# Kernel optimization log

Measured on AMD Instinct MI355X. Metric: run time of the kernel, lower is better.

## Reference

```python
import jax, jax.numpy as jnp
import numpy as np

B, N, C, H = 8, 1024, 768, 12
D = C // H  # head dim
SCALE = D ** -0.5


def setup_inputs() -> dict:
    key = jax.random.key(0)
    ks = jax.random.split(key, 5)
    return {
        "x": jax.random.normal(ks[0], (B, N, C), dtype=jnp.float32),
        "W_qkv": jax.random.normal(ks[1], (C, 3 * C), dtype=jnp.float32) * (C ** -0.5),
        "b_qkv": jax.random.normal(ks[2], (3 * C,), dtype=jnp.float32) * 0.02,
        "W_proj": jax.random.normal(ks[3], (C, C), dtype=jnp.float32) * (C ** -0.5),
        "b_proj": jax.random.normal(ks[4], (C,), dtype=jnp.float32) * 0.02,
    }


def reference(x, W_qkv, b_qkv, W_proj, b_proj):
    b, n, c = x.shape
    qkv = x @ W_qkv + b_qkv                      # [B,N,3C]
    # rearrange 'b n (k h c) -> k b h n c'
    qkv = qkv.reshape(b, n, 3, H, D).transpose(2, 0, 3, 1, 4)
    q, k, v = qkv[0] * SCALE, qkv[1], qkv[2]     # each [B,H,N,D]
    p = jax.nn.softmax(jnp.einsum('bhnd,bhmd->bhnm', q, k), axis=-1)
    o = jnp.einsum('bhnm,bhmd->bhnd', p, v)      # [B,H,N,D]
    o = o.transpose(0, 2, 1, 3).reshape(b, n, c)  # 'b h n c -> b n (h c)'
    return o @ W_proj + b_proj
```

## Files before the change

### kernel.cpp

```cpp
#include <hip/hip_runtime.h>


typedef short  bf16x8_t __attribute__((ext_vector_type(8)));
typedef float  f32x4_t  __attribute__((ext_vector_type(4)));

static __device__ __forceinline__ unsigned short f2bf(float f) {
    union { float f; unsigned u; } v; v.f = f;
    unsigned r = v.u + 0x7fffu + ((v.u >> 16) & 1u);
    return (unsigned short)(r >> 16);
}

typedef __attribute__((address_space(1))) const unsigned gas_u32;
typedef __attribute__((address_space(3))) unsigned las_u32;
static __device__ __forceinline__ void gload16(const void* g, void* l) {
    __builtin_amdgcn_global_load_lds((gas_u32*)g, (las_u32*)l, 16, 0, 0);
}

#define WAIT0 asm volatile("s_waitcnt vmcnt(0)" ::: "memory")
#define BAR   __builtin_amdgcn_s_barrier()

#define STAGE_TILE(DST, SRC, K0, NP, NT)                                   \
    _Pragma("unroll")                                                      \
    for (int p_ = 0; p_ < NP; ++p_) {                                      \
        const int base_ = p_*NT + wb;                                      \
        const int i_ = base_ + lane;                                       \
        const int row_ = i_ >> 3;                                          \
        const int cb_ = ((i_ & 7) ^ (row_ & 7)) * 8;                       \
        gload16((SRC) + (size_t)row_*768 + (K0) + cb_, &(DST)[base_*8]);   \
    }

#define COMPUTE_P(AS, BS)                                                  \
    {                                                                      \
        bf16x8_t a_[2][2], b_[2][4];                                       \
        _Pragma("unroll")                                                  \
        for (int ks_ = 0; ks_ < 2; ++ks_) {                                \
            _Pragma("unroll")                                              \
            for (int m_ = 0; m_ < 2; ++m_) {                               \
                const int ra_ = wm*32 + m_*16 + l15;                       \
                a_[ks_][m_] = *(const bf16x8_t*)&(AS)[ra_*64 + ((ks_*4 + lhi) ^ (ra_ & 7))*8]; \
            }                                                              \
            _Pragma("unroll")                                              \
            for (int n_ = 0; n_ < 4; ++n_) {                               \
                const int rb_ = wn*64 + n_*16 + l15;                       \
                b_[ks_][n_] = *(const bf16x8_t*)&(BS)[rb_*64 + ((ks_*4 + lhi) ^ (rb_ & 7))*8]; \
            }                                                              \
        }                                                                  \
        _Pragma("unroll")                                                  \
        for (int m_ = 0; m_ < 2; ++m_)                                     \
            _Pragma("unroll")                                              \
            for (int n_ = 0; n_ < 4; ++n_) {                               \
                acc[m_][n_] = __builtin_amdgcn_mfma_f32_16x16x32_bf16(a_[0][m_], b_[0][n_], acc[m_][n_], 0, 0, 0); \
                acc[m_][n_] = __builtin_amdgcn_mfma_f32_16x16x32_bf16(a_[1][m_], b_[1][n_], acc[m_][n_], 0, 0, 0); \
            }                                                              \
    }

#define COMPUTE_Q2(AS, BS)                                                 \
    {                                                                      \
        bf16x8_t a_[2][4], b_[2][2];                                       \
        _Pragma("unroll")                                                  \
        for (int ks_ = 0; ks_ < 2; ++ks_) {                                \
            _Pragma("unroll")                                              \
            for (int m_ = 0; m_ < 4; ++m_) {                               \
                const int ra_ = wm*64 + m_*16 + l15;                       \
                a_[ks_][m_] = *(const bf16x8_t*)&(AS)[ra_*64 + ((ks_*4 + lhi) ^ (ra_ & 7))*8]; \
            }                                                              \
            _Pragma("unroll")                                              \
            for (int n_ = 0; n_ < 2; ++n_) {                               \
                const int rb_ = wn*32 + n_*16 + l15;                       \
                b_[ks_][n_] = *(const bf16x8_t*)&(BS)[rb_*64 + ((ks_*4 + lhi) ^ (rb_ & 7))*8]; \
            }                                                              \
        }                                                                  \
        _Pragma("unroll")                                                  \
        for (int m_ = 0; m_ < 4; ++m_)                                     \
            _Pragma("unroll")                                              \
            for (int n_ = 0; n_ < 2; ++n_) {                               \
                acc[m_][n_] = __builtin_amdgcn_mfma_f32_16x16x32_bf16(a_[0][m_], b_[0][n_], acc[m_][n_], 0, 0, 0); \
                acc[m_][n_] = __builtin_amdgcn_mfma_f32_16x16x32_bf16(a_[1][m_], b_[1][n_], acc[m_][n_], 0, 0, 0); \
            }                                                              \
    }

__global__ __launch_bounds__(256) void convert_x(
    const float* __restrict__ src, unsigned short* __restrict__ dst)
{
    const int i = blockIdx.x * 256 + threadIdx.x;
    const float4 v = ((const float4*)src)[i];
    ushort4 o; o.x = f2bf(v.x); o.y = f2bf(v.y); o.z = f2bf(v.z); o.w = f2bf(v.w);
    ((ushort4*)dst)[i] = o;
}

__global__ __launch_bounds__(256) void transpose_cvt(
    const float* __restrict__ src, unsigned short* __restrict__ dst, int R, int C)
{
    __shared__ unsigned short tile[32][33];
    const int tx = threadIdx.x & 31, ty = threadIdx.x >> 5;
    const int bx = blockIdx.x, by = blockIdx.y;
    #pragma unroll
    for (int j = 0; j < 32; j += 8)
        tile[ty + j][tx] = f2bf(src[(size_t)(by*32 + ty + j) * C + bx*32 + tx]);
    __syncthreads();
    #pragma unroll
    for (int j = 0; j < 32; j += 8)
        dst[(size_t)(bx*32 + ty + j) * R + by*32 + tx] = tile[tx][ty + j];
}

__global__ __launch_bounds__(256, 6) void gemm_qkv_bf16(
    const unsigned short* __restrict__ A, const unsigned short* __restrict__ Bt,
    const float* __restrict__ bias,
    unsigned short* __restrict__ q, unsigned short* __restrict__ kO,
    unsigned short* __restrict__ vT)
{
    __shared__ unsigned short As[128*64];
    __shared__ unsigned short Bs[64*64];
    const int tid = threadIdx.x;
    const int id = blockIdx.x;
    const int xcd = id & 7, r = id >> 3;
    const int nb = r >> 3;
    const int mb = (r & 7) * 8 + xcd;
    const int n0 = nb * 64, m0 = mb * 128;

    const int lane = tid & 63, w = tid >> 6;
    const int l15 = lane & 15, lhi = lane >> 4;
    const int wm = w >> 1, wn = w & 1;
    const int wb = tid & 192;

    const unsigned short* Ab = A  + (size_t)m0 * 768;
    const unsigned short* Bb = Bt + (size_t)n0 * 768;

    f32x4_t acc[4][2] = {};

    #pragma unroll 1
    for (int t = 0; t < 12; ++t) {
        STAGE_TILE(As, Ab, t*64, 4, 256)
        STAGE_TILE(Bs, Bb, t*64, 2, 256)
        WAIT0; BAR;
        COMPUTE_Q2(As, Bs)
        BAR;
    }

    #pragma unroll
    for (int n = 0; n < 2; ++n) {
        const int gcol = n0 + wn*32 + n*16 + l15;
        const int kk = gcol / 768;
        const int rr = gcol - kk*768;
        const int h  = rr >> 6, d = rr & 63;
        const float bv = bias[gcol];
        const float sc = (kk == 0) ? 0.125f : 1.0f;
        #pragma unroll
        for (int m = 0; m < 4; ++m) {
            const int grow_base = m0 + wm*64 + m*16 + lhi*4;
            #pragma unroll
            for (int reg = 0; reg < 4; ++reg) {
                const int grow = grow_base + reg;
                const int bb = grow >> 10, seq = grow & 1023;
                const unsigned short ov = f2bf((acc[m][n][reg] + bv) * sc);
                const size_t bh = (size_t)bb*12 + h;
                if (kk == 0)      q [ (bh*1024 + seq)*64 + d ] = ov;
                else if (kk == 1) kO[ (bh*1024 + seq)*64 + d ] = ov;
                else              vT[ (bh*64 + d)*1024 + seq ] = ov;
            }
        }
    }
}

__global__ __launch_bounds__(512, 6) void attn2(
    const unsigned short* __restrict__ q, const unsigned short* __restrict__ k,
    const unsigned short* __restrict__ vT, unsigned short* __restrict__ obuf)
{
    __shared__ unsigned short Ks[64 * 72];
    __shared__ unsigned short Vs[64 * 72];
    __shared__ unsigned short P[8][16 * 72];
    const int tid = threadIdx.x;
    const int id = blockIdx.x;
    const int swz = (id & 7) * 96 + (id >> 3);
    const int qt = swz & 7, bh = swz >> 3;

    const int lane = tid & 63, w = tid >> 6;
    const int l15 = lane & 15, lhi = lane >> 4;
    const unsigned short* qp = q  + (size_t)bh * 65536;
    const unsigned short* kp = k  + (size_t)bh * 65536;
    const unsigned short* vp = vT + (size_t)bh * 65536;

    bf16x8_t qf[2];
    const int qrow = qt*128 + w*16 + l15;
    #pragma unroll
    for (int ks = 0; ks < 2; ++ks)
        qf[ks] = *(const bf16x8_t*)(qp + (size_t)qrow*64 + ks*32 + lhi*8);

    f32x4_t acco[4] = {};
    float lsum[4] = {0.f, 0.f, 0.f, 0.f};
    unsigned short* Pw = P[w];

    const int r8 = tid >> 3, cb = (tid & 7) * 8;
    bf16x8_t kr, vr;
    kr = *(const bf16x8_t*)(kp + (size_t)r8*64 + cb);
    vr = *(const bf16x8_t*)(vp + (size_t)r8*1024 + cb);
    *(bf16x8_t*)&Ks[r8*72 + cb] = kr;
    *(bf16x8_t*)&Vs[r8*72 + cb] = vr;

    for (int kt = 0; kt < 16; ++kt) {
        __syncthreads();
        if (kt < 15) {
            kr = *(const bf16x8_t*)(kp + (size_t)((kt+1)*64 + r8)*64 + cb);
            vr = *(const bf16x8_t*)(vp + (size_t)r8*1024 + (kt+1)*64 + cb);
        }

        f32x4_t accs[4] = {};
        __builtin_amdgcn_s_setprio(1);
        #pragma unroll
        for (int c = 0; c < 4; ++c)
            #pragma unroll
            for (int ks = 0; ks < 2; ++ks) {
                bf16x8_t kf = *(const bf16x8_t*)&Ks[(c*16 + l15)*72 + ks*32 + lhi*8];
                accs[c] = __builtin_amdgcn_mfma_f32_16x16x32_bf16(qf[ks], kf, accs[c], 0, 0, 0);
            }
        __builtin_amdgcn_s_setprio(0);

        #pragma unroll
        for (int c = 0; c < 4; ++c)
            #pragma unroll
            for (int r = 0; r < 4; ++r) {
                const float pv = __expf(accs[c][r]);
                lsum[r] += pv;
                Pw[(lhi*4 + r)*72 + c*16 + l15] = f2bf(pv);
            }

        bf16x8_t pf[2];
        #pragma unroll
        for (int ks = 0; ks < 2; ++ks)
            pf[ks] = *(const bf16x8_t*)&Pw[l15*72 + ks*32 + lhi*8];
        __builtin_amdgcn_s_setprio(1);
        #pragma unroll
        for (int n = 0; n < 4; ++n)
            #pragma unroll
            for (int ks = 0; ks < 2; ++ks) {
                bf16x8_t vf = *(const bf16x8_t*)&Vs[(n*16 + l15)*72 + ks*32 + lhi*8];
                acco[n] = __builtin_amdgcn_mfma_f32_16x16x32_bf16(pf[ks], vf, acco[n], 0, 0, 0);
            }
        __builtin_amdgcn_s_setprio(0);

        __syncthreads();
        if (kt < 15) {
            *(bf16x8_t*)&Ks[r8*72 + cb] = kr;
            *(bf16x8_t*)&Vs[r8*72 + cb] = vr;
        }
    }

    #pragma unroll
    for (int r = 0; r < 4; ++r)
        #pragma unroll
        for (int off = 1; off <= 8; off <<= 1)
            lsum[r] += __shfl_xor(lsum[r], off, 64);

    const int b = bh / 12, h = bh % 12;
    #pragma unroll
    for (int n = 0; n < 4; ++n)
        #pragma unroll
        for (int r = 0; r < 4; ++r) {
            const int seq = qt*128 + w*16 + lhi*4 + r;
            obuf[((size_t)(b*1024 + seq))*768 + h*64 + n*16 + l15] = f2bf(acco[n][r] / lsum[r]);
        }
}

__global__ __launch_bounds__(256, 6) void gemm_proj_bf16(
    const unsigned short* __restrict__ A, const unsigned short* __restrict__ Bt,
    const float* __restrict__ bias, float* __restrict__ out)
{
    __shared__ unsigned short As[64*64];
    __shared__ unsigned short Bs[128*64];
    const int tid = threadIdx.x;
    const int id = blockIdx.x;
    const int swz = (id & 7) * 96 + (id >> 3);
    const int n0 = (swz % 6) * 128, m0 = (swz / 6) * 64;

    const int lane = tid & 63, w = tid >> 6;
    const int l15 = lane & 15, lhi = lane >> 4;
    const int wm = w >> 1, wn = w & 1;
    const int wb = tid & 192;

    const unsigned short* Ab = A  + (size_t)m0 * 768;
    const unsigned short* Bb = Bt + (size_t)n0 * 768;

    f32x4_t acc[2][4] = {};

    #pragma unroll 1
    for (int t = 0; t < 12; ++t) {
        STAGE_TILE(As, Ab, t*64, 2, 256)
        STAGE_TILE(Bs, Bb, t*64, 4, 256)
        WAIT0; BAR;
        COMPUTE_P(As, Bs)
        BAR;
    }

    #pragma unroll
    for (int n = 0; n < 4; ++n) {
        const int gcol = n0 + wn*64 + n*16 + l15;
        const float bv = bias[gcol];
        #pragma unroll
        for (int m = 0; m < 2; ++m) {
            const int grow_base = m0 + wm*32 + m*16 + lhi*4;
            #pragma unroll
            for (int reg = 0; reg < 4; ++reg)
                out[(size_t)(grow_base + reg)*768 + gcol] = acc[m][n][reg] + bv;
        }
    }
}

extern "C" void kernel_launch(void* const* d_in, const int* in_sizes, int n_in,
                              void* d_out, int out_size, void* d_ws, size_t ws_size,
                              hipStream_t stream) {
    const float* x     = (const float*)d_in[0];
    const float* Wqkv  = (const float*)d_in[1];
    const float* bqkv  = (const float*)d_in[2];
    const float* Wproj = (const float*)d_in[3];
    const float* bproj = (const float*)d_in[4];
    float* out = (float*)d_out;
    unsigned short* ws = (unsigned short*)d_ws;

    unsigned short* xb    = ws;
    unsigned short* obuf  = ws;
    unsigned short* wqt   = ws + 6291456u;
    unsigned short* wpt   = ws + 8060928u;
    unsigned short* qb    = ws + 8650752u;
    unsigned short* kb    = ws + 14942208u;
    unsigned short* vTb   = ws + 21233664u;

    convert_x     <<<6144, 256, 0, stream>>>(x, xb);
    transpose_cvt <<<dim3(72, 24), 256, 0, stream>>>(Wqkv, wqt, 768, 2304);
    transpose_cvt <<<dim3(24, 24), 256, 0, stream>>>(Wproj, wpt, 768, 768);
    gemm_qkv_bf16 <<<2304, 256, 0, stream>>>(xb, wqt, bqkv, qb, kb, vTb);
    attn2         <<<768,  512, 0, stream>>>(qb, kb, vTb, obuf);
    gemm_proj_bf16<<<768,  256, 0, stream>>>(obuf, wpt, bproj, out);
}
```

Measured before the change: 123.3 us.

## Process 32 query rows per wave in attention and vectorize V-transpose stores

The attention kernel now gives each wave two 16-row query groups (256 rows per block) and halves the grid to 384 blocks. Each K and V fragment read from LDS then feeds two MFMAs, and every staged K/V tile is reused across twice as many queries, cutting LDS and global traffic per unit of work. The cost is more registers and LDS, with launch bounds lowered to 4, and fewer blocks than before on a 256-CU device, which may leave the machine less evenly loaded. Separately, the QKV GEMM epilogue writes the transposed V output as one 4-element vector store instead of four scalar stores.

```diff
diff --git a/kernel.cpp b/kernel.cpp
--- a/kernel.cpp
+++ b/kernel.cpp
@@ -148,31 +148,37 @@
         #pragma unroll
         for (int m = 0; m < 4; ++m) {
             const int grow_base = m0 + wm*64 + m*16 + lhi*4;
-            #pragma unroll
-            for (int reg = 0; reg < 4; ++reg) {
-                const int grow = grow_base + reg;
-                const int bb = grow >> 10, seq = grow & 1023;
-                const unsigned short ov = f2bf((acc[m][n][reg] + bv) * sc);
-                const size_t bh = (size_t)bb*12 + h;
-                if (kk == 0)      q [ (bh*1024 + seq)*64 + d ] = ov;
-                else if (kk == 1) kO[ (bh*1024 + seq)*64 + d ] = ov;
-                else              vT[ (bh*64 + d)*1024 + seq ] = ov;
+            const int bb = grow_base >> 10, seq0 = grow_base & 1023;
+            const size_t bh = (size_t)bb*12 + h;
+            ushort4 o4;
+            o4.x = f2bf((acc[m][n][0] + bv) * sc);
+            o4.y = f2bf((acc[m][n][1] + bv) * sc);
+            o4.z = f2bf((acc[m][n][2] + bv) * sc);
+            o4.w = f2bf((acc[m][n][3] + bv) * sc);
+            if (kk == 2) {
+                *(ushort4*)(vT + (bh*64 + d)*1024 + seq0) = o4;
+            } else {
+                unsigned short* dst = (kk == 0) ? q : kO;
+                dst[(bh*1024 + seq0 + 0)*64 + d] = o4.x;
+                dst[(bh*1024 + seq0 + 1)*64 + d] = o4.y;
+                dst[(bh*1024 + seq0 + 2)*64 + d] = o4.z;
+                dst[(bh*1024 + seq0 + 3)*64 + d] = o4.w;
             }
         }
     }
 }
 
-__global__ __launch_bounds__(512, 6) void attn2(
+__global__ __launch_bounds__(512, 4) void attn2(
     const unsigned short* __restrict__ q, const unsigned short* __restrict__ k,
     const unsigned short* __restrict__ vT, unsigned short* __restrict__ obuf)
 {
     __shared__ unsigned short Ks[64 * 72];
     __shared__ unsigned short Vs[64 * 72];
-    __shared__ unsigned short P[8][16 * 72];
+    __shared__ unsigned short P[8][32 * 72];
     const int tid = threadIdx.x;
     const int id = blockIdx.x;
-    const int swz = (id & 7) * 96 + (id >> 3);
-    const int qt = swz & 7, bh = swz >> 3;
+    const int swz = (id & 7) * 48 + (id >> 3);
+    const int qt = swz & 3, bh = swz >> 2;
 
     const int lane = tid & 63, w = tid >> 6;
     const int l15 = lane & 15, lhi = lane >> 4;
@@ -180,14 +186,15 @@
     const unsigned short* kp = k  + (size_t)bh * 65536;
     const unsigned short* vp = vT + (size_t)bh * 65536;
 
-    bf16x8_t qf[2];
-    const int qrow = qt*128 + w*16 + l15;
-    #pragma unroll
-    for (int ks = 0; ks < 2; ++ks)
-        qf[ks] = *(const bf16x8_t*)(qp + (size_t)qrow*64 + ks*32 + lhi*8);
-
-    f32x4_t acco[4] = {};
-    float lsum[4] = {0.f, 0.f, 0.f, 0.f};
+    bf16x8_t qf[2][2];
+    #pragma unroll
+    for (int g = 0; g < 2; ++g)
+        #pragma unroll
+        for (int ks = 0; ks < 2; ++ks)
+            qf[g][ks] = *(const bf16x8_t*)(qp + (size_t)(qt*256 + w*32 + g*16 + l15)*64 + ks*32 + lhi*8);
+
+    f32x4_t acco[2][4] = {};
+    float lsum[2][4] = {};
     unsigned short* Pw = P[w];
 
     const int r8 = tid >> 3, cb = (tid & 7) * 8;
@@ -204,37 +211,45 @@
             vr = *(const bf16x8_t*)(vp + (size_t)r8*1024 + (kt+1)*64 + cb);
         }
 
-        f32x4_t accs[4] = {};
+        f32x4_t accs[2][4] = {};
         __builtin_amdgcn_s_setprio(1);
         #pragma unroll
         for (int c = 0; c < 4; ++c)
             #pragma unroll
             for (int ks = 0; ks < 2; ++ks) {
                 bf16x8_t kf = *(const bf16x8_t*)&Ks[(c*16 + l15)*72 + ks*32 + lhi*8];
-                accs[c] = __builtin_amdgcn_mfma_f32_16x16x32_bf16(qf[ks], kf, accs[c], 0, 0, 0);
+                #pragma unroll
+                for (int g = 0; g < 2; ++g)
+                    accs[g][c] = __builtin_amdgcn_mfma_f32_16x16x32_bf16(qf[g][ks], kf, accs[g][c], 0, 0, 0);
             }
         __builtin_amdgcn_s_setprio(0);
 
         #pragma unroll
-        for (int c = 0; c < 4; ++c)
-            #pragma unroll
-            for (int r = 0; r < 4; ++r) {
-                const float pv = __expf(accs[c][r]);
-                lsum[r] += pv;
-                Pw[(lhi*4 + r)*72 + c*16 + l15] = f2bf(pv);
-            }
-
-        bf16x8_t pf[2];
-        #pragma unroll
-        for (int ks = 0; ks < 2; ++ks)
-            pf[ks] = *(const bf16x8_t*)&Pw[l15*72 + ks*32 + lhi*8];
+        for (int g = 0; g < 2; ++g)
+            #pragma unroll
+            for (int c = 0; c < 4; ++c)
+                #pragma unroll
+                for (int r = 0; r < 4; ++r) {
+                    const float pv = __expf(accs[g][c][r]);
+                    lsum[g][r] += pv;
+                    Pw[(g*16 + lhi*4 + r)*72 + c*16 + l15] = f2bf(pv);
+                }
+
+        bf16x8_t pf[2][2];
+        #pragma unroll
+        for (int g = 0; g < 2; ++g)
+            #pragma unroll
+            for (int ks = 0; ks < 2; ++ks)
+                pf[g][ks] = *(const bf16x8_t*)&Pw[(g*16 + l15)*72 + ks*32 + lhi*8];
         __builtin_amdgcn_s_setprio(1);
         #pragma unroll
         for (int n = 0; n < 4; ++n)
             #pragma unroll
             for (int ks = 0; ks < 2; ++ks) {
                 bf16x8_t vf = *(const bf16x8_t*)&Vs[(n*16 + l15)*72 + ks*32 + lhi*8];
-                acco[n] = __builtin_amdgcn_mfma_f32_16x16x32_bf16(pf[ks], vf, acco[n], 0, 0, 0);
+                #pragma unroll
+                for (int g = 0; g < 2; ++g)
+                    acco[g][n] = __builtin_amdgcn_mfma_f32_16x16x32_bf16(pf[g][ks], vf, acco[g][n], 0, 0, 0);
             }
         __builtin_amdgcn_s_setprio(0);
 
@@ -246,19 +261,24 @@
     }
 
     #pragma unroll
-    for (int r = 0; r < 4; ++r)
-        #pragma unroll
-        for (int off = 1; off <= 8; off <<= 1)
-            lsum[r] += __shfl_xor(lsum[r], off, 64);
+    for (int g = 0; g < 2; ++g)
+        #pragma unroll
+        for (int r = 0; r < 4; ++r)
+            #pragma unroll
+            for (int off = 1; off <= 8; off <<= 1)
+                lsum[g][r] += __shfl_xor(lsum[g][r], off, 64);
 
     const int b = bh / 12, h = bh % 12;
     #pragma unroll
-    for (int n = 0; n < 4; ++n)
-        #pragma unroll
-        for (int r = 0; r < 4; ++r) {
-            const int seq = qt*128 + w*16 + lhi*4 + r;
-            obuf[((size_t)(b*1024 + seq))*768 + h*64 + n*16 + l15] = f2bf(acco[n][r] / lsum[r]);
-        }
+    for (int g = 0; g < 2; ++g)
+        #pragma unroll
+        for (int n = 0; n < 4; ++n)
+            #pragma unroll
+            for (int r = 0; r < 4; ++r) {
+                const int seq = qt*256 + w*32 + g*16 + lhi*4 + r;
+                obuf[((size_t)(b*1024 + seq))*768 + h*64 + n*16 + l15] =
+                    f2bf(acco[g][n][r] / lsum[g][r]);
+            }
 }
 
 __global__ __launch_bounds__(256, 6) void gemm_proj_bf16(
@@ -328,6 +348,6 @@
     transpose_cvt <<<dim3(72, 24), 256, 0, stream>>>(Wqkv, wqt, 768, 2304);
     transpose_cvt <<<dim3(24, 24), 256, 0, stream>>>(Wproj, wpt, 768, 768);
     gemm_qkv_bf16 <<<2304, 256, 0, stream>>>(xb, wqt, bqkv, qb, kb, vTb);
-    attn2         <<<768,  512, 0, stream>>>(qb, kb, vTb, obuf);
+    attn2         <<<384,  512, 0, stream>>>(qb, kb, vTb, obuf);
     gemm_proj_bf16<<<768,  256, 0, stream>>>(obuf, wpt, bproj, out);
 }
```

New measurement: 119.4 us. 1.03x faster.
